# Optimization experiments

Hardware: AMD Instinct MI355X
Metric: run time of the kernel (lower is better)

## Reference

```python
import jax, jax.numpy as jnp
import numpy as np

EMBED_DIM = 584
HEADS = 8
HEAD_SIZE = EMBED_DIM // HEADS  # 73
CTX = 200


def setup_inputs() -> dict:
    key = jax.random.key(0)
    ks = jax.random.split(key, 6)
    B, T = 256, 200
    x = jax.random.normal(ks[0], (B, T, EMBED_DIM), dtype=jnp.float32)
    s = 1.0 / np.sqrt(EMBED_DIM)
    # per-head q/k/v Linear(EMBED_DIM, HEAD_SIZE, bias=False) weights, stacked: [H, hs, E]
    Wq = jax.random.uniform(ks[1], (HEADS, HEAD_SIZE, EMBED_DIM), jnp.float32, -s, s)
    Wk = jax.random.uniform(ks[2], (HEADS, HEAD_SIZE, EMBED_DIM), jnp.float32, -s, s)
    Wv = jax.random.uniform(ks[3], (HEADS, HEAD_SIZE, EMBED_DIM), jnp.float32, -s, s)
    Wo = jax.random.uniform(ks[4], (EMBED_DIM, EMBED_DIM), jnp.float32, -s, s)
    bo = jax.random.uniform(ks[5], (EMBED_DIM,), jnp.float32, -s, s)
    return {"x": x, "Wq": Wq, "Wk": Wk, "Wv": Wv, "Wo": Wo, "bo": bo}


def reference(x, Wq, Wk, Wv, Wo, bo):
    B, T, C = x.shape  # C == EMBED_DIM
    # per-head projections, batched: [B, H, T, hs]
    q = jnp.einsum('bte,hfe->bhtf', x, Wq)
    k = jnp.einsum('bte,hfe->bhtf', x, Wk)
    v = jnp.einsum('bte,hfe->bhtf', x, Wv)
    # NOTE: original scales by EMBED_DIM**-0.5 (C), not head_size**-0.5
    scores = jnp.einsum('bhtf,bhsf->bhts', q, k) * (C ** -0.5)
    causal = jnp.tril(jnp.ones((T, T), dtype=bool))
    scores = jnp.where(causal, scores, -jnp.inf)
    w = jax.nn.softmax(scores, axis=-1)
    out = jnp.einsum('bhts,bhsf->bhtf', w, v)  # [B,H,T,hs]
    out = out.transpose(0, 2, 1, 3).reshape(B, T, C)  # concat heads on last dim
    return out @ Wo.T + bo
```

## Files before the change

### kernel.cpp

```cpp
#include <hip/hip_runtime.h>

typedef __bf16 bf16x8 __attribute__((ext_vector_type(8)));
typedef __bf16 bf16x4 __attribute__((ext_vector_type(4)));
typedef float f32x4 __attribute__((ext_vector_type(4)));

#define EMBED 584
#define KP 608
#define HEADS 8
#define HS 73
#define HSQ 80
#define CTX 200
#define NBATCH 256
#define MROWS 51200
#define NQKV 1752

#define PSS 232

__device__ __forceinline__ void gld_lds16(__bf16* lds, const __bf16* g) {
  __builtin_amdgcn_global_load_lds(
      (const __attribute__((address_space(1))) void*)g,
      (__attribute__((address_space(3))) void*)lds, 16, 0, 0);
}

__global__ __launch_bounds__(256) void cvt_x(const float* __restrict__ x,
                                             __bf16* __restrict__ out) {
  int i = blockIdx.x * 256 + threadIdx.x;
  int r = i / 76, slot = i - r * 76;
  int col = slot * 8;
  bf16x8 o8 = {};
  if (col < EMBED) {
    const float4* s4 = (const float4*)(x + (size_t)r * EMBED + col);
    float4 f0 = s4[0], f1 = s4[1];
    o8[0] = (__bf16)f0.x; o8[1] = (__bf16)f0.y; o8[2] = (__bf16)f0.z; o8[3] = (__bf16)f0.w;
    o8[4] = (__bf16)f1.x; o8[5] = (__bf16)f1.y; o8[6] = (__bf16)f1.z; o8[7] = (__bf16)f1.w;
  }
  *(bf16x8*)(out + (size_t)r * KP + col) = o8;
}

__global__ __launch_bounds__(256) void pack_w(const float* __restrict__ Wq,
                                              const float* __restrict__ Wk,
                                              const float* __restrict__ Wv,
                                              const float* __restrict__ Wo,
                                              __bf16* __restrict__ out) {
  int i = blockIdx.x * 256 + threadIdx.x;
  if (i >= 2336 * 76) return;
  int r = i / 76, slot = i - r * 76;
  int col = slot * 8;
  bf16x8 o8 = {};
  if (col < EMBED) {
    const float* src = r < 584  ? Wq + (size_t)r * EMBED
                     : r < 1168 ? Wk + (size_t)(r - 584) * EMBED
                     : r < 1752 ? Wv + (size_t)(r - 1168) * EMBED
                                : Wo + (size_t)(r - 1752) * EMBED;
    const float4* s4 = (const float4*)(src + col);
    float4 f0 = s4[0], f1 = s4[1];
    o8[0] = (__bf16)f0.x; o8[1] = (__bf16)f0.y; o8[2] = (__bf16)f0.z; o8[3] = (__bf16)f0.w;
    o8[4] = (__bf16)f1.x; o8[5] = (__bf16)f1.y; o8[6] = (__bf16)f1.z; o8[7] = (__bf16)f1.w;
  }
  *(bf16x8*)(out + (size_t)r * KP + col) = o8;
}

__global__ __launch_bounds__(256) void zero_pads(__bf16* __restrict__ qb,
                                                 __bf16* __restrict__ kb,
                                                 __bf16* __restrict__ vb) {
  int bh = blockIdx.x;
  bf16x8 z = {};
  __bf16* qp = qb + (size_t)bh * 16000;
  __bf16* kp = kb + (size_t)bh * 16000;
  __bf16* vp = vb + (size_t)bh * 16000;
  for (int i = threadIdx.x; i < 575; i += 256) {
    if (i < 200)      *(bf16x8*)&qp[i * 80 + 72] = z;
    else if (i < 400) *(bf16x8*)&kp[(i - 200) * 80 + 72] = z;
    else              *(bf16x8*)&vp[14600 + (i - 400) * 8] = z;
  }
}

__global__ __launch_bounds__(512, 4) void gemm_qkv(const __bf16* __restrict__ A,
                                                   const __bf16* __restrict__ Bm,
                                                   __bf16* __restrict__ Q,
                                                   __bf16* __restrict__ Ko,
                                                   __bf16* __restrict__ V) {
  __shared__ __bf16 As[3][8192];
  __shared__ __bf16 Bs[3][4096];
  int tid = threadIdx.x;
  int id = blockIdx.x;
  int idp = (id & 7) * 350 + (id >> 3);
  int bm = idp / 14, bn = idp - bm * 14;
  int wid = tid >> 6, lane = tid & 63;
  int wm = (wid & 3) * 64, wn = (wid >> 2) * 64;
  int lr = lane & 15, lq = lane >> 4;
  int sw = (((lane & 3) ^ ((lane >> 2) & 3))) * 8;
  const __bf16* aB = A  + (size_t)(bm * 256 + wid * 32 + (lane >> 2)) * KP + sw;
  const __bf16* bB = Bm + (size_t)(bn * 128 + wid * 16 + (lane >> 2)) * KP + sw;
  f32x4 acc[4][4] = {};

#define STAGE_QKV(buf, kt)                                        \
  do {                                                            \
    int k0_ = (kt) * 32;                                          \
    gld_lds16(As[buf] + wid * 1024,       aB + k0_);              \
    gld_lds16(As[buf] + wid * 1024 + 512, aB + 16 * KP + k0_);    \
    gld_lds16(Bs[buf] + wid * 512,        bB + k0_);              \
  } while (0)

  STAGE_QKV(0, 0);
  STAGE_QKV(1, 1);
  int cxr = (lq ^ (lr & 3)) * 8;
#pragma unroll
  for (int kt = 0; kt < 19; ++kt) {
    if (kt < 18) asm volatile("s_waitcnt vmcnt(3)" ::: "memory");
    else         asm volatile("s_waitcnt vmcnt(0)" ::: "memory");
    __builtin_amdgcn_s_barrier();
    if (kt + 2 < 19) STAGE_QKV((kt + 2) % 3, kt + 2);
    const __bf16* Ac = As[kt % 3];
    const __bf16* Bc = Bs[kt % 3];
    bf16x8 af[4], bfr[4];
#pragma unroll
    for (int i = 0; i < 4; ++i)
      af[i] = *(const bf16x8*)&Ac[(wm + i * 16 + lr) * 32 + cxr];
#pragma unroll
    for (int j = 0; j < 4; ++j)
      bfr[j] = *(const bf16x8*)&Bc[(wn + j * 16 + lr) * 32 + cxr];
    __builtin_amdgcn_s_setprio(1);
#pragma unroll
    for (int i = 0; i < 4; ++i)
#pragma unroll
      for (int j = 0; j < 4; ++j)
        acc[i][j] = __builtin_amdgcn_mfma_f32_16x16x32_bf16(af[i], bfr[j], acc[i][j], 0, 0, 0);
    __builtin_amdgcn_s_setprio(0);
  }
#undef STAGE_QKV
  int whichj[4], ojv[4];
  __bf16* Pj[4];
  bool okj[4];
#pragma unroll
  for (int j = 0; j < 4; ++j) {
    int n = bn * 128 + wn + j * 16 + lr;
    okj[j] = (n < NQKV);
    int nn = okj[j] ? n : 0;
    int which = nn / EMBED;
    int rem = nn - which * EMBED;
    int hh = rem / HS;
    int f = rem - hh * HS;
    whichj[j] = which;
    ojv[j] = (which == 2) ? (hh * 16000 + f * 200) : (hh * 16000 + f);
    Pj[j] = (which == 0) ? Q : (which == 1) ? Ko : V;
  }
#pragma unroll
  for (int i = 0; i < 4; ++i) {
    int m0 = bm * 256 + wm + i * 16 + lq * 4;
    int bb = m0 / CTX;
    int tt = m0 - bb * CTX;
    int a_qk = bb * 128000 + tt * 80;
    int a_v  = bb * 128000 + tt;
#pragma unroll
    for (int j = 0; j < 4; ++j) {
      if (!okj[j]) continue;
      if (whichj[j] == 2) {
        bf16x4 v4;
#pragma unroll
        for (int r = 0; r < 4; ++r) v4[r] = (__bf16)acc[i][j][r];
        *(bf16x4*)&Pj[j][a_v + ojv[j]] = v4;
      } else {
        int base = a_qk + ojv[j];
#pragma unroll
        for (int r = 0; r < 4; ++r)
          Pj[j][base + r * 80] = (__bf16)acc[i][j][r];
      }
    }
  }
}

__global__ __launch_bounds__(256, 4) void attn_kernel(const __bf16* __restrict__ q,
                                                      const __bf16* __restrict__ k,
                                                      const __bf16* __restrict__ v,
                                                      __bf16* __restrict__ o) {
  __shared__ __align__(16) __bf16 Ps[4][16 * PSS];
  int tid = threadIdx.x;
  int bh = blockIdx.x;
  int b = bh >> 3, h = bh & 7;
  const __bf16* qg = q + (size_t)bh * 16000;
  const __bf16* kg = k + (size_t)bh * 16000;
  const __bf16* vg = v + (size_t)bh * 16000;

  if (h == 0) {
    bf16x8 z = {};
    for (int i = tid; i < CTX * 3; i += 256) {
      int t = i / 3, seg = i - t * 3;
      *(bf16x8*)&o[((size_t)(b * CTX + t)) * KP + EMBED + seg * 8] = z;
    }
  }

  int wid = tid >> 6, lane = tid & 63;
  int lr = lane & 15, g = lane >> 4;
  __bf16* Pw = Ps[wid];
  const float scale = 0.04138029443264672f;

  int sl[4];
  sl[0] = 12 - wid;
  sl[1] = (wid < 3) ? 6 + wid : 5;
  sl[2] = (wid < 3) ? 1 + wid : 4;
  sl[3] = (wid < 3) ? -1 : 0;

#pragma unroll
  for (int si = 0; si < 4; ++si) {
    int s = sl[si];
    if (s < 0) continue;
    int row0 = s * 16;
    bf16x8 qf[3];
    qf[0] = *(const bf16x8*)&qg[(size_t)(row0 + lr) * HSQ + g * 8];
    qf[1] = *(const bf16x8*)&qg[(size_t)(row0 + lr) * HSQ + 32 + g * 8];
    qf[2] = (g < 2) ? *(const bf16x8*)&qg[(size_t)(row0 + lr) * HSQ + 64 + g * 8]
                    : bf16x8{};
    float sc[13][4];
#pragma unroll
    for (int nt = 0; nt < 13; ++nt) {
      if (nt > s) continue;
      f32x4 acc = {};
#pragma unroll
      for (int kc = 0; kc < 3; ++kc) {
        bf16x8 kf = *(const bf16x8*)&kg[(size_t)(nt * 16 + lr) * HSQ + kc * 32 + g * 8];
        acc = __builtin_amdgcn_mfma_f32_16x16x32_bf16(qf[kc], kf, acc, 0, 0, 0);
      }
#pragma unroll
      for (int r = 0; r < 4; ++r) {
        float val = acc[r] * scale;
        if (nt == s && lr > g * 4 + r) val = -1e30f;
        if (nt * 16 + lr >= CTX) val = -1e30f;
        sc[nt][r] = val;
      }
    }
    float mr[4], rs[4];
#pragma unroll
    for (int r = 0; r < 4; ++r) {
      float m = -1e30f;
#pragma unroll
      for (int nt = 0; nt < 13; ++nt)
        if (nt <= s) m = fmaxf(m, sc[nt][r]);
      mr[r] = m;
    }
#pragma unroll
    for (int off = 8; off; off >>= 1)
#pragma unroll
      for (int r = 0; r < 4; ++r)
        mr[r] = fmaxf(mr[r], __shfl_xor(mr[r], off, 64));
#pragma unroll
    for (int r = 0; r < 4; ++r) {
      float ssum = 0.f;
#pragma unroll
      for (int nt = 0; nt < 13; ++nt) {
        if (nt > s) continue;
        sc[nt][r] = __expf(sc[nt][r] - mr[r]);
        ssum += sc[nt][r];
      }
      rs[r] = ssum;
    }
#pragma unroll
    for (int off = 8; off; off >>= 1)
#pragma unroll
      for (int r = 0; r < 4; ++r) rs[r] += __shfl_xor(rs[r], off, 64);
#pragma unroll
    for (int nt = 0; nt < 13; ++nt) {
      if (nt > s) continue;
#pragma unroll
      for (int r = 0; r < 4; ++r)
        Pw[(g * 4 + r) * PSS + nt * 16 + lr] = (__bf16)sc[nt][r];
    }
    if ((s & 1) == 0) {
#pragma unroll
      for (int r = 0; r < 4; ++r)
        Pw[(g * 4 + r) * PSS + (s + 1) * 16 + lr] = (__bf16)0.f;
    }
    f32x4 ov[5];
#pragma unroll
    for (int nt = 0; nt < 5; ++nt) ov[nt] = f32x4{0.f, 0.f, 0.f, 0.f};
#pragma unroll
    for (int kc = 0; kc < 7; ++kc) {
      if (kc > s / 2) continue;
      bf16x8 pf = *(const bf16x8*)&Pw[lr * PSS + kc * 32 + g * 8];
#pragma unroll
      for (int nt = 0; nt < 5; ++nt) {
        bf16x8 vf = *(const bf16x8*)&vg[(size_t)(nt * 16 + lr) * CTX + kc * 32 + g * 8];
        ov[nt] = __builtin_amdgcn_mfma_f32_16x16x32_bf16(pf, vf, ov[nt], 0, 0, 0);
      }
    }
    float inv[4];
#pragma unroll
    for (int r = 0; r < 4; ++r) inv[r] = 1.0f / rs[r];
#pragma unroll
    for (int nt = 0; nt < 5; ++nt) {
      int f = nt * 16 + lr;
      if (f < HS) {
#pragma unroll
        for (int r = 0; r < 4; ++r) {
          int t = row0 + g * 4 + r;
          if (t < CTX)
            o[((size_t)(b * CTX + t)) * KP + h * HS + f] =
                (__bf16)(ov[nt][r] * inv[r]);
        }
      }
    }
  }
}

__global__ __launch_bounds__(512, 4) void gemm_out(const __bf16* __restrict__ A,
                                                   const __bf16* __restrict__ Bm,
                                                   const float* __restrict__ bias,
                                                   float* __restrict__ C) {
  constexpr int N = EMBED;
  __shared__ __bf16 As[3][8192];
  __shared__ __bf16 Bs[3][4096];
  int tid = threadIdx.x;
  int id = blockIdx.x;
  int idp = (id & 7) * 125 + (id >> 3);
  int bm = idp / 5, bn = idp - bm * 5;
  int wid = tid >> 6, lane = tid & 63;
  int wm = (wid & 3) * 64, wn = (wid >> 2) * 64;
  int lr = lane & 15, lq = lane >> 4;
  int sw = (((lane & 3) ^ ((lane >> 2) & 3))) * 8;
  const __bf16* aB = A  + (size_t)(bm * 256 + wid * 32 + (lane >> 2)) * KP + sw;
  const __bf16* bB = Bm + (size_t)(bn * 128 + wid * 16 + (lane >> 2)) * KP + sw;
  f32x4 acc[4][4] = {};

#define STAGE_OUT(buf, kt)                                        \
  do {                                                            \
    int k0_ = (kt) * 32;                                          \
    gld_lds16(As[buf] + wid * 1024,       aB + k0_);              \
    gld_lds16(As[buf] + wid * 1024 + 512, aB + 16 * KP + k0_);    \
    gld_lds16(Bs[buf] + wid * 512,        bB + k0_);              \
  } while (0)

  STAGE_OUT(0, 0);
  STAGE_OUT(1, 1);
  int cxr = (lq ^ (lr & 3)) * 8;
#pragma unroll
  for (int kt = 0; kt < 19; ++kt) {
    if (kt < 18) asm volatile("s_waitcnt vmcnt(3)" ::: "memory");
    else         asm volatile("s_waitcnt vmcnt(0)" ::: "memory");
    __builtin_amdgcn_s_barrier();
    if (kt + 2 < 19) STAGE_OUT((kt + 2) % 3, kt + 2);
    const __bf16* Ac = As[kt % 3];
    const __bf16* Bc = Bs[kt % 3];
    bf16x8 af[4], bfr[4];
#pragma unroll
    for (int i = 0; i < 4; ++i)
      af[i] = *(const bf16x8*)&Ac[(wm + i * 16 + lr) * 32 + cxr];
#pragma unroll
    for (int j = 0; j < 4; ++j)
      bfr[j] = *(const bf16x8*)&Bc[(wn + j * 16 + lr) * 32 + cxr];
    __builtin_amdgcn_s_setprio(1);
#pragma unroll
    for (int i = 0; i < 4; ++i)
#pragma unroll
      for (int j = 0; j < 4; ++j)
        acc[i][j] = __builtin_amdgcn_mfma_f32_16x16x32_bf16(af[i], bfr[j], acc[i][j], 0, 0, 0);
    __builtin_amdgcn_s_setprio(0);
  }
#undef STAGE_OUT
#pragma unroll
  for (int i = 0; i < 4; ++i) {
    int m = bm * 256 + wm + i * 16 + lq * 4;
#pragma unroll
    for (int j = 0; j < 4; ++j) {
      int n = bn * 128 + wn + j * 16 + lr;
      if (n < N) {
        float bval = bias[n];
#pragma unroll
        for (int r = 0; r < 4; ++r)
          C[(size_t)(m + r) * N + n] = acc[i][j][r] + bval;
      }
    }
  }
}

extern "C" void kernel_launch(void* const* d_in, const int* in_sizes, int n_in,
                              void* d_out, int out_size, void* d_ws, size_t ws_size,
                              hipStream_t stream) {
  const float* x  = (const float*)d_in[0];
  const float* Wq = (const float*)d_in[1];
  const float* Wk = (const float*)d_in[2];
  const float* Wv = (const float*)d_in[3];
  const float* Wo = (const float*)d_in[4];
  const float* bo = (const float*)d_in[5];
  float* out = (float*)d_out;

  __bf16* wcat = (__bf16*)d_ws;
  __bf16* vb   = wcat + 1420288ULL;
  __bf16* qb   = vb + 32768000ULL;
  __bf16* kb   = qb + 32768000ULL;
  __bf16* xb   = kb + 32768000ULL;
  __bf16* ab   = xb;

  cvt_x<<<15200, 256, 0, stream>>>(x, xb);
  pack_w<<<694, 256, 0, stream>>>(Wq, Wk, Wv, Wo, wcat);
  zero_pads<<<2048, 256, 0, stream>>>(qb, kb, vb);
  gemm_qkv<<<2800, 512, 0, stream>>>(xb, wcat, qb, kb, vb);
  attn_kernel<<<2048, 256, 0, stream>>>(qb, kb, vb, ab);
  gemm_out<<<1000, 512, 0, stream>>>(ab, wcat + 1752ULL * KP, bo, out);
}
```

Baseline: 630.9 us.

## Fuse fp32-to-bf16 conversion of x into QKV GEMM loader; merge prep kernels

Removes the separate cvt_x pass by having gemm_qkv read fp32 x directly into registers, convert to bf16, and write the swizzled tile into LDS (now double-buffered for A). The pack_w and zero_pads kernels are merged into one launch. This avoids writing and re-reading a bf16 copy of x and cuts two launches. In exchange, A loads go through registers with a full vmcnt(0) wait each iteration, which weakens overlap, and each x tile is reread in fp32 by 14 column blocks.

```diff
diff --git a/kernel.cpp b/kernel.cpp
--- a/kernel.cpp
+++ b/kernel.cpp
@@ -22,65 +22,52 @@
       (__attribute__((address_space(3))) void*)lds, 16, 0, 0);
 }
 
-__global__ __launch_bounds__(256) void cvt_x(const float* __restrict__ x,
-                                             __bf16* __restrict__ out) {
-  int i = blockIdx.x * 256 + threadIdx.x;
-  int r = i / 76, slot = i - r * 76;
-  int col = slot * 8;
-  bf16x8 o8 = {};
-  if (col < EMBED) {
-    const float4* s4 = (const float4*)(x + (size_t)r * EMBED + col);
-    float4 f0 = s4[0], f1 = s4[1];
-    o8[0] = (__bf16)f0.x; o8[1] = (__bf16)f0.y; o8[2] = (__bf16)f0.z; o8[3] = (__bf16)f0.w;
-    o8[4] = (__bf16)f1.x; o8[5] = (__bf16)f1.y; o8[6] = (__bf16)f1.z; o8[7] = (__bf16)f1.w;
-  }
-  *(bf16x8*)(out + (size_t)r * KP + col) = o8;
-}
-
-__global__ __launch_bounds__(256) void pack_w(const float* __restrict__ Wq,
-                                              const float* __restrict__ Wk,
-                                              const float* __restrict__ Wv,
-                                              const float* __restrict__ Wo,
-                                              __bf16* __restrict__ out) {
-  int i = blockIdx.x * 256 + threadIdx.x;
-  if (i >= 2336 * 76) return;
-  int r = i / 76, slot = i - r * 76;
-  int col = slot * 8;
-  bf16x8 o8 = {};
-  if (col < EMBED) {
-    const float* src = r < 584  ? Wq + (size_t)r * EMBED
-                     : r < 1168 ? Wk + (size_t)(r - 584) * EMBED
-                     : r < 1752 ? Wv + (size_t)(r - 1168) * EMBED
-                                : Wo + (size_t)(r - 1752) * EMBED;
-    const float4* s4 = (const float4*)(src + col);
-    float4 f0 = s4[0], f1 = s4[1];
-    o8[0] = (__bf16)f0.x; o8[1] = (__bf16)f0.y; o8[2] = (__bf16)f0.z; o8[3] = (__bf16)f0.w;
-    o8[4] = (__bf16)f1.x; o8[5] = (__bf16)f1.y; o8[6] = (__bf16)f1.z; o8[7] = (__bf16)f1.w;
-  }
-  *(bf16x8*)(out + (size_t)r * KP + col) = o8;
-}
-
-__global__ __launch_bounds__(256) void zero_pads(__bf16* __restrict__ qb,
-                                                 __bf16* __restrict__ kb,
-                                                 __bf16* __restrict__ vb) {
-  int bh = blockIdx.x;
+__global__ __launch_bounds__(256) void pack_w_zero(const float* __restrict__ Wq,
+                                                   const float* __restrict__ Wk,
+                                                   const float* __restrict__ Wv,
+                                                   const float* __restrict__ Wo,
+                                                   __bf16* __restrict__ out,
+                                                   __bf16* __restrict__ qb,
+                                                   __bf16* __restrict__ kb,
+                                                   __bf16* __restrict__ vb) {
+  int bid = blockIdx.x, tid = threadIdx.x;
+  if (bid < 694) {
+    int i = bid * 256 + tid;
+    if (i < 2336 * 76) {
+      int r = i / 76, slot = i - r * 76;
+      int col = slot * 8;
+      bf16x8 o8 = {};
+      if (col < EMBED) {
+        const float* src = r < 584  ? Wq + (size_t)r * EMBED
+                         : r < 1168 ? Wk + (size_t)(r - 584) * EMBED
+                         : r < 1752 ? Wv + (size_t)(r - 1168) * EMBED
+                                    : Wo + (size_t)(r - 1752) * EMBED;
+        const float4* s4 = (const float4*)(src + col);
+        float4 f0 = s4[0], f1 = s4[1];
+        o8[0] = (__bf16)f0.x; o8[1] = (__bf16)f0.y; o8[2] = (__bf16)f0.z; o8[3] = (__bf16)f0.w;
+        o8[4] = (__bf16)f1.x; o8[5] = (__bf16)f1.y; o8[6] = (__bf16)f1.z; o8[7] = (__bf16)f1.w;
+      }
+      *(bf16x8*)(out + (size_t)r * KP + col) = o8;
+    }
+  }
+  int bh = bid;
   bf16x8 z = {};
   __bf16* qp = qb + (size_t)bh * 16000;
   __bf16* kp = kb + (size_t)bh * 16000;
   __bf16* vp = vb + (size_t)bh * 16000;
-  for (int i = threadIdx.x; i < 575; i += 256) {
+  for (int i = tid; i < 575; i += 256) {
     if (i < 200)      *(bf16x8*)&qp[i * 80 + 72] = z;
     else if (i < 400) *(bf16x8*)&kp[(i - 200) * 80 + 72] = z;
     else              *(bf16x8*)&vp[14600 + (i - 400) * 8] = z;
   }
 }
 
-__global__ __launch_bounds__(512, 4) void gemm_qkv(const __bf16* __restrict__ A,
+__global__ __launch_bounds__(512, 4) void gemm_qkv(const float* __restrict__ X,
                                                    const __bf16* __restrict__ Bm,
                                                    __bf16* __restrict__ Q,
                                                    __bf16* __restrict__ Ko,
                                                    __bf16* __restrict__ V) {
-  __shared__ __bf16 As[3][8192];
+  __shared__ __bf16 As[2][8192];
   __shared__ __bf16 Bs[3][4096];
   int tid = threadIdx.x;
   int id = blockIdx.x;
@@ -89,29 +76,57 @@
   int wid = tid >> 6, lane = tid & 63;
   int wm = (wid & 3) * 64, wn = (wid >> 2) * 64;
   int lr = lane & 15, lq = lane >> 4;
-  int sw = (((lane & 3) ^ ((lane >> 2) & 3))) * 8;
-  const __bf16* aB = A  + (size_t)(bm * 256 + wid * 32 + (lane >> 2)) * KP + sw;
+  int arow = wid * 32 + (lane >> 1);
+  int r3 = arow & 3;
+  int c80 = (lane & 1) * 2;
+  int s0 = ((c80) ^ r3) * 8;
+  int s1 = ((c80 + 1) ^ r3) * 8;
+  const float* xrow = X + (size_t)(bm * 256 + arow) * EMBED;
+  int sw = ((lane & 3) ^ ((lane >> 2) & 3)) * 8;
   const __bf16* bB = Bm + (size_t)(bn * 128 + wid * 16 + (lane >> 2)) * KP + sw;
   f32x4 acc[4][4] = {};
-
-#define STAGE_QKV(buf, kt)                                        \
-  do {                                                            \
-    int k0_ = (kt) * 32;                                          \
-    gld_lds16(As[buf] + wid * 1024,       aB + k0_);              \
-    gld_lds16(As[buf] + wid * 1024 + 512, aB + 16 * KP + k0_);    \
-    gld_lds16(Bs[buf] + wid * 512,        bB + k0_);              \
+  float4 ar0, ar1, ar2, ar3;
+
+#define LOAD_A(kt)                                                      \
+  do {                                                                  \
+    if ((kt) < 18) {                                                    \
+      const float* p_ = xrow + (kt) * 32;                               \
+      ar0 = *(const float4*)(p_ + s0);                                  \
+      ar1 = *(const float4*)(p_ + s0 + 4);                              \
+      ar2 = *(const float4*)(p_ + s1);                                  \
+      ar3 = *(const float4*)(p_ + s1 + 4);                              \
+    } else {                                                            \
+      float4 z_ = {0.f, 0.f, 0.f, 0.f};                                 \
+      ar0 = (s0 == 0) ? *(const float4*)(xrow + 576) : z_;              \
+      ar1 = (s0 == 0) ? *(const float4*)(xrow + 580) : z_;              \
+      ar2 = (s1 == 0) ? *(const float4*)(xrow + 576) : z_;              \
+      ar3 = (s1 == 0) ? *(const float4*)(xrow + 580) : z_;              \
+    }                                                                   \
   } while (0)
-
-  STAGE_QKV(0, 0);
-  STAGE_QKV(1, 1);
+#define CVT_WRITE(buf)                                                  \
+  do {                                                                  \
+    bf16x8 w0, w1;                                                      \
+    w0[0]=(__bf16)ar0.x; w0[1]=(__bf16)ar0.y; w0[2]=(__bf16)ar0.z; w0[3]=(__bf16)ar0.w; \
+    w0[4]=(__bf16)ar1.x; w0[5]=(__bf16)ar1.y; w0[6]=(__bf16)ar1.z; w0[7]=(__bf16)ar1.w; \
+    w1[0]=(__bf16)ar2.x; w1[1]=(__bf16)ar2.y; w1[2]=(__bf16)ar2.z; w1[3]=(__bf16)ar2.w; \
+    w1[4]=(__bf16)ar3.x; w1[5]=(__bf16)ar3.y; w1[6]=(__bf16)ar3.z; w1[7]=(__bf16)ar3.w; \
+    *(bf16x8*)&As[buf][arow * 32 + c80 * 8] = w0;                       \
+    *(bf16x8*)&As[buf][arow * 32 + c80 * 8 + 8] = w1;                   \
+  } while (0)
+#define STAGE_B(buf, kt) gld_lds16(Bs[buf] + wid * 512, bB + (kt) * 32)
+
+  LOAD_A(0);
+  STAGE_B(0, 0);
+  asm volatile("s_waitcnt vmcnt(0)" ::: "memory");
+  CVT_WRITE(0);
+  LOAD_A(1);
+  STAGE_B(1, 1);
   int cxr = (lq ^ (lr & 3)) * 8;
 #pragma unroll
   for (int kt = 0; kt < 19; ++kt) {
-    if (kt < 18) asm volatile("s_waitcnt vmcnt(3)" ::: "memory");
-    else         asm volatile("s_waitcnt vmcnt(0)" ::: "memory");
+    asm volatile("s_waitcnt lgkmcnt(0)" ::: "memory");
     __builtin_amdgcn_s_barrier();
-    if (kt + 2 < 19) STAGE_QKV((kt + 2) % 3, kt + 2);
-    const __bf16* Ac = As[kt % 3];
+    const __bf16* Ac = As[kt & 1];
     const __bf16* Bc = Bs[kt % 3];
     bf16x8 af[4], bfr[4];
 #pragma unroll
@@ -127,8 +142,15 @@
       for (int j = 0; j < 4; ++j)
         acc[i][j] = __builtin_amdgcn_mfma_f32_16x16x32_bf16(af[i], bfr[j], acc[i][j], 0, 0, 0);
     __builtin_amdgcn_s_setprio(0);
-  }
-#undef STAGE_QKV
+    if (kt < 18) {
+      asm volatile("s_waitcnt vmcnt(0)" ::: "memory");
+      CVT_WRITE((kt + 1) & 1);
+      if (kt + 2 < 19) { LOAD_A(kt + 2); STAGE_B((kt + 2) % 3, kt + 2); }
+    }
+  }
+#undef LOAD_A
+#undef CVT_WRITE
+#undef STAGE_B
   int whichj[4], ojv[4];
   __bf16* Pj[4];
   bool okj[4];
@@ -387,13 +409,10 @@
   __bf16* vb   = wcat + 1420288ULL;
   __bf16* qb   = vb + 32768000ULL;
   __bf16* kb   = qb + 32768000ULL;
-  __bf16* xb   = kb + 32768000ULL;
-  __bf16* ab   = xb;
-
-  cvt_x<<<15200, 256, 0, stream>>>(x, xb);
-  pack_w<<<694, 256, 0, stream>>>(Wq, Wk, Wv, Wo, wcat);
-  zero_pads<<<2048, 256, 0, stream>>>(qb, kb, vb);
-  gemm_qkv<<<2800, 512, 0, stream>>>(xb, wcat, qb, kb, vb);
+  __bf16* ab   = kb + 32768000ULL;
+
+  pack_w_zero<<<2048, 256, 0, stream>>>(Wq, Wk, Wv, Wo, wcat, qb, kb, vb);
+  gemm_qkv<<<2800, 512, 0, stream>>>(x, wcat, qb, kb, vb);
   attn_kernel<<<2048, 256, 0, stream>>>(qb, kb, vb, ab);
   gemm_out<<<1000, 512, 0, stream>>>(ab, wcat + 1752ULL * KP, bo, out);
 }
```

After: 755.0 us. 1.2x slower.
